# Kernel tuning notes

Measured on AMD Instinct MI355X. Metric: run time of the kernel, lower is better.

Reference implementation:

```python
import jax, jax.numpy as jnp
import numpy as np

D_MODEL = 1024
N_HEADS = 16
HEAD_DIM = D_MODEL // N_HEADS


def setup_inputs() -> dict:
    key = jax.random.key(0)
    k_x, k_wqkv, k_bqkv, k_wp, k_bp = jax.random.split(key, 5)
    B, N = 2, 2048
    x = jax.random.normal(k_x, (B, N, D_MODEL), dtype=jnp.float32)
    s = 1.0 / np.sqrt(D_MODEL)
    w_qkv = jax.random.uniform(k_wqkv, (D_MODEL, 3 * D_MODEL), jnp.float32, -s, s)
    b_qkv = jax.random.uniform(k_bqkv, (3 * D_MODEL,), jnp.float32, -s, s)
    w_proj = jax.random.uniform(k_wp, (D_MODEL, D_MODEL), jnp.float32, -s, s)
    b_proj = jax.random.uniform(k_bp, (D_MODEL,), jnp.float32, -s, s)
    return {"x": x, "w_qkv": w_qkv, "b_qkv": b_qkv, "w_proj": w_proj, "b_proj": b_proj}


def reference(x, w_qkv, b_qkv, w_proj, b_proj):
    B, N, C = x.shape
    scale = HEAD_DIM ** (-0.5)
    qkv = x @ w_qkv + b_qkv  # [B, N, 3C]
    qkv = qkv.reshape(B, N, 3, N_HEADS, HEAD_DIM).transpose(2, 0, 3, 1, 4)
    q, k, v = qkv[0], qkv[1], qkv[2]  # each [B, H, N, Dh]
    p = jnp.einsum('bhnd,bhmd->bhnm', q, k) * scale  # [B, H, N, N]
    p = jax.nn.softmax(p, axis=-1)
    o = jnp.einsum('bhnm,bhmd->bhnd', p, v)  # [B, H, N, Dh]
    o = o.transpose(0, 2, 1, 3).reshape(B, N, C)
    return o @ w_proj + b_proj
```

## Files before the change

### kernel.cpp

```cpp
#include <hip/hip_runtime.h>


typedef short v8s __attribute__((ext_vector_type(8)));
typedef float v4f __attribute__((ext_vector_type(4)));
typedef unsigned int v4u __attribute__((ext_vector_type(4)));

#define QSCALE 0.18033688011112042f

#if defined(__has_builtin)
# if __has_builtin(__builtin_amdgcn_exp2f)
#  define EXP2(x) __builtin_amdgcn_exp2f(x)
# endif
#endif
#ifndef EXP2
static __device__ __forceinline__ float exp2_asm(float x) {
    float r;
    asm volatile("v_exp_f32 %0, %1\n\ts_nop 1" : "=v"(r) : "v"(x));
    return r;
}
# define EXP2(x) exp2_asm(x)
#endif

static __device__ __forceinline__ unsigned short f2bf_fast(float f) {
    union { float f; unsigned int u; } a;
    a.f = f;
    return (unsigned short)((a.u + 0x8000u) >> 16);
}

static __device__ __forceinline__ unsigned int pack_bf16(float lo, float hi) {
    union { float f; unsigned int u; } a, b;
    a.f = lo; b.f = hi;
    return __builtin_amdgcn_perm(b.u + 0x8000u, a.u + 0x8000u, 0x07060302u);
}

#define GLD16(g, l) __builtin_amdgcn_global_load_lds( \
    (const __attribute__((address_space(1))) unsigned int*)(g), \
    (__attribute__((address_space(3))) unsigned int*)(l), 16, 0, 0)

__global__ __launch_bounds__(256) void prep(const float* __restrict__ x,
                                            unsigned short* __restrict__ xb,
                                            const float* __restrict__ w_qkv,
                                            unsigned short* __restrict__ wqkvt,
                                            const float* __restrict__ w_proj,
                                            unsigned short* __restrict__ wprojt) {
    __shared__ float tile[32][33];
    const int bid = blockIdx.x, tid = threadIdx.x;
    if (bid < 4096) {
        int i = bid * 256 + tid;
        float4 f = ((const float4*)x)[i];
        ushort4 o;
        o.x = f2bf_fast(f.x); o.y = f2bf_fast(f.y); o.z = f2bf_fast(f.z); o.w = f2bf_fast(f.w);
        ((ushort4*)xb)[i] = o;
        return;
    }
    const float* w; unsigned short* wt; int R, C, bx, by;
    if (bid < 7168) { w = w_qkv; wt = wqkvt; R = 1024; C = 3072;
                      int t = bid - 4096; bx = t % 96; by = t / 96; }
    else            { w = w_proj; wt = wprojt; R = 1024; C = 1024;
                      int t = bid - 7168; bx = t & 31; by = t >> 5; }
    const int tx = tid & 31, ty = tid >> 5;
    const int c0 = bx * 32, r0 = by * 32;
#pragma unroll
    for (int j = 0; j < 32; j += 8)
        tile[ty + j][tx] = w[(r0 + ty + j) * C + c0 + tx];
    __syncthreads();
#pragma unroll
    for (int j = 0; j < 32; j += 8)
        wt[(c0 + ty + j) * R + r0 + tx] = f2bf_fast(tile[tx][ty + j]);
}

__global__ __launch_bounds__(256) void gemm_bt(const unsigned short* __restrict__ A,
                                               const unsigned short* __restrict__ Bt,
                                               const float* __restrict__ bias,
                                               int M, int N, int K, int mode,
                                               unsigned short* __restrict__ qo,
                                               unsigned short* __restrict__ ko,
                                               unsigned short* __restrict__ vto,
                                               float* __restrict__ outp) {
    __shared__ unsigned short Sh[17408];
    const int tid = threadIdx.x;
    const int wave = tid >> 6, lane = tid & 63;
    const int quad = lane >> 4, l16 = lane & 15;
    const int bm = blockIdx.y * 128, bn = blockIdx.x * 128;
    const int wm = (wave >> 1) * 64, wn = (wave & 1) * 64;
    const int rsw = (quad ^ ((l16 >> 1) & 3)) << 3;

    v4f acc[4][4];
#pragma unroll
    for (int i = 0; i < 4; i++)
#pragma unroll
        for (int j = 0; j < 4; j++) acc[i][j] = (v4f){0.f, 0.f, 0.f, 0.f};

#define GSTAGE(b, kk) do { \
    _Pragma("unroll") \
    for (int i_ = 0; i_ < 2; i_++) { \
        int c_ = i_ * 256 + tid; \
        int r_ = c_ >> 2; \
        int g_ = ((c_ & 3) ^ ((r_ >> 1) & 3)) << 3; \
        GLD16(&A[(bm + r_) * K + (kk) + g_], &Sh[((b) << 12) + (c_ << 3)]); \
        GLD16(&Bt[(bn + r_) * K + (kk) + g_], &Sh[8192 + ((b) << 12) + (c_ << 3)]); \
    } } while (0)

#define GCOMP(b) do { \
    v8s af_[4], bf_[4]; \
    _Pragma("unroll") \
    for (int mi_ = 0; mi_ < 4; mi_++) \
        af_[mi_] = *(const v8s*)&Sh[((b) << 12) + (wm + mi_ * 16 + l16) * 32 + rsw]; \
    _Pragma("unroll") \
    for (int ni_ = 0; ni_ < 4; ni_++) \
        bf_[ni_] = *(const v8s*)&Sh[8192 + ((b) << 12) + (wn + ni_ * 16 + l16) * 32 + rsw]; \
    _Pragma("unroll") \
    for (int mi_ = 0; mi_ < 4; mi_++) \
        _Pragma("unroll") \
        for (int ni_ = 0; ni_ < 4; ni_++) \
            acc[mi_][ni_] = __builtin_amdgcn_mfma_f32_16x16x32_bf16( \
                af_[mi_], bf_[ni_], acc[mi_][ni_], 0, 0, 0); \
    } while (0)

    GSTAGE(0, 0);
    for (int k0 = 0; k0 < K; k0 += 64) {
        __syncthreads();
        if (k0 + 32 < K) GSTAGE(1, k0 + 32);
        GCOMP(0);
        __syncthreads();
        if (k0 + 64 < K) GSTAGE(0, k0 + 64);
        GCOMP(1);
    }
#undef GSTAGE
#undef GCOMP

    if (mode == 1) {
#pragma unroll
        for (int mi = 0; mi < 4; mi++)
#pragma unroll
            for (int ni = 0; ni < 4; ni++) {
                int col = bn + wn + ni * 16 + l16;
                float bv = bias[col];
                int row0 = bm + wm + mi * 16 + quad * 4;
#pragma unroll
                for (int r = 0; r < 4; r++)
                    outp[(row0 + r) * N + col] = acc[mi][ni][r] + bv;
            }
    } else if (bn < 2048) {
        const int isq = (bn < 1024);
        unsigned short* dst = isq ? qo : ko;
        const float sc = isq ? QSCALE : 1.0f;
#pragma unroll
        for (int mi = 0; mi < 4; mi++)
#pragma unroll
            for (int ni = 0; ni < 4; ni++) {
                int col = bn + wn + ni * 16 + l16;
                float bv = bias[col];
                int rem = col & 1023;
                int h = rem >> 6, dh = rem & 63;
                int row0 = bm + wm + mi * 16 + quad * 4;
                int b = row0 >> 11, n = row0 & 2047;
                unsigned short* p = &dst[(((b * 16 + h) << 11) + n) * 64 + dh];
                p[0]   = f2bf_fast((acc[mi][ni][0] + bv) * sc);
                p[64]  = f2bf_fast((acc[mi][ni][1] + bv) * sc);
                p[128] = f2bf_fast((acc[mi][ni][2] + bv) * sc);
                p[192] = f2bf_fast((acc[mi][ni][3] + bv) * sc);
            }
    } else {
        __syncthreads();
#pragma unroll
        for (int mi = 0; mi < 4; mi++)
#pragma unroll
            for (int ni = 0; ni < 4; ni++) {
                int col = bn + wn + ni * 16 + l16;
                float bv = bias[col];
                ushort4 pk;
                pk.x = f2bf_fast(acc[mi][ni][0] + bv);
                pk.y = f2bf_fast(acc[mi][ni][1] + bv);
                pk.z = f2bf_fast(acc[mi][ni][2] + bv);
                pk.w = f2bf_fast(acc[mi][ni][3] + bv);
                *(ushort4*)&Sh[(wn + ni * 16 + l16) * 136 +
                               wm + ((mi >> 1) * 32) + quad * 8 + ((mi & 1) * 4)] = pk;
            }
        __syncthreads();
        const int b = bm >> 11, n_base = bm & 2047;
#pragma unroll
        for (int j = 0; j < 8; j++) {
            int idx = j * 256 + tid;
            int Lcol = idx >> 4, rc = idx & 15;
            int rem = (bn + Lcol) & 1023;
            int h = rem >> 6, dh = rem & 63;
            *(int4*)&vto[((((b * 16 + h) * 64 + dh) << 11) + n_base + rc * 8)] =
                *(const int4*)&Sh[Lcol * 136 + rc * 8];
        }
    }
}

__global__ __launch_bounds__(256, 4) void attn(const unsigned short* __restrict__ q,
                                               const unsigned short* __restrict__ k,
                                               const unsigned short* __restrict__ vt,
                                               unsigned short* __restrict__ o) {
    __shared__ unsigned short Ks[2][64 * 64];
    __shared__ unsigned short Vs[2][64 * 64];
    const int tid = threadIdx.x;
    const int wave = tid >> 6, lane = tid & 63;
    const int quad = lane >> 4, l16 = lane & 15;
    const int sw = l16 & 7;

    const int id = blockIdx.y * 32 + blockIdx.x;
    const int bh = (id & 7) * 4 + ((id >> 3) & 3);
    const int wq0 = (id >> 5) * 64 + wave * 16;
    const int rowg = bh * 2048 + wq0;

    v8s qf[2];
#pragma unroll
    for (int half = 0; half < 2; half++)
        qf[half] = *(const v8s*)&q[(rowg + l16) * 64 + half * 32 + quad * 8];

    v8s onef;
#pragma unroll
    for (int j = 0; j < 8; j++) onef[j] = (short)0x3F80;

    v4f oacc[4];
    v4f lacc = (v4f){0.f, 0.f, 0.f, 0.f};
#pragma unroll
    for (int dt = 0; dt < 4; dt++) oacc[dt] = (v4f){0.f, 0.f, 0.f, 0.f};

    const unsigned short* kbase = k + (((long)bh << 11) * 64);
    const unsigned short* vbase = vt + (((long)bh * 64) << 11);

#define STAGE(buf, n0s) do { \
    _Pragma("unroll") \
    for (int i_ = 0; i_ < 2; i_++) { \
        int c_ = i_ * 256 + tid; \
        int r_ = c_ >> 3; \
        int chs_ = ((c_ & 7) ^ (r_ & 7)) << 3; \
        GLD16(&kbase[((n0s) + r_) * 64 + chs_], &Ks[buf][c_ << 3]); \
        GLD16(&vbase[(r_ << 11) + (n0s) + chs_], &Vs[buf][c_ << 3]); \
    } } while (0)

    auto tile = [&](const unsigned short* Kc, const unsigned short* Vc) {
        v4f s[4];
        __builtin_amdgcn_s_setprio(1);
#pragma unroll
        for (int ni = 0; ni < 4; ni++) {
            int rowk = (ni * 16 + l16) * 64;
            v8s kf0 = *(const v8s*)&Kc[rowk + ((quad ^ sw) << 3)];
            v8s kf1 = *(const v8s*)&Kc[rowk + (((4 + quad) ^ sw) << 3)];
            v4f z = (v4f){0.f, 0.f, 0.f, 0.f};
            z = __builtin_amdgcn_mfma_f32_16x16x32_bf16(kf0, qf[0], z, 0, 0, 0);
            z = __builtin_amdgcn_mfma_f32_16x16x32_bf16(kf1, qf[1], z, 0, 0, 0);
            s[ni] = z;
        }
        __builtin_amdgcn_s_setprio(0);

        v8s af[2];
#pragma unroll
        for (int t = 0; t < 2; t++) {
            v4u w;
            w[0] = pack_bf16(EXP2(s[2 * t][0]),     EXP2(s[2 * t][1]));
            w[1] = pack_bf16(EXP2(s[2 * t][2]),     EXP2(s[2 * t][3]));
            w[2] = pack_bf16(EXP2(s[2 * t + 1][0]), EXP2(s[2 * t + 1][1]));
            w[3] = pack_bf16(EXP2(s[2 * t + 1][2]), EXP2(s[2 * t + 1][3]));
            union { v4u u; v8s s8; } cv;
            cv.u = w;
            af[t] = cv.s8;
        }

        __builtin_amdgcn_s_setprio(1);
#pragma unroll
        for (int dt = 0; dt < 4; dt++) {
            int rowv = (dt * 16 + l16) * 64;
            v8s vf0 = *(const v8s*)&Vc[rowv + ((quad ^ sw) << 3)];
            v8s vf1 = *(const v8s*)&Vc[rowv + (((4 + quad) ^ sw) << 3)];
            oacc[dt] = __builtin_amdgcn_mfma_f32_16x16x32_bf16(af[0], vf0, oacc[dt], 0, 0, 0);
            oacc[dt] = __builtin_amdgcn_mfma_f32_16x16x32_bf16(af[1], vf1, oacc[dt], 0, 0, 0);
        }
        lacc = __builtin_amdgcn_mfma_f32_16x16x32_bf16(af[0], onef, lacc, 0, 0, 0);
        lacc = __builtin_amdgcn_mfma_f32_16x16x32_bf16(af[1], onef, lacc, 0, 0, 0);
        __builtin_amdgcn_s_setprio(0);
    };

    STAGE(0, 0);
    for (int n0 = 0; n0 < 2048; n0 += 128) {
        __syncthreads();
        if (n0 + 64 < 2048) STAGE(1, n0 + 64);
        tile(Ks[0], Vs[0]);
        __syncthreads();
        if (n0 + 128 < 2048) STAGE(0, n0 + 128);
        tile(Ks[1], Vs[1]);
    }
#undef STAGE

    const int b = bh >> 4, h = bh & 15;
#pragma unroll
    for (int r = 0; r < 4; r++) {
        float linv = 1.0f / lacc[r];
        int n = wq0 + quad * 4 + r;
#pragma unroll
        for (int dt = 0; dt < 4; dt++)
            o[(b * 2048 + n) * 1024 + h * 64 + dt * 16 + l16] =
                f2bf_fast(oacc[dt][r] * linv);
    }
}

extern "C" void kernel_launch(void* const* d_in, const int* in_sizes, int n_in,
                              void* d_out, int out_size, void* d_ws, size_t ws_size,
                              hipStream_t stream) {
    const float* x      = (const float*)d_in[0];
    const float* w_qkv  = (const float*)d_in[1];
    const float* b_qkv  = (const float*)d_in[2];
    const float* w_proj = (const float*)d_in[3];
    const float* b_proj = (const float*)d_in[4];
    float* outp = (float*)d_out;

    unsigned short* ws     = (unsigned short*)d_ws;
    unsigned short* xb     = ws;
    unsigned short* wqkvt  = ws + 4194304;
    unsigned short* wprojt = wqkvt + 3145728;
    unsigned short* qws    = wprojt + 1048576;
    unsigned short* kws    = qws + 4194304;
    unsigned short* vtws   = kws + 4194304;
    unsigned short* ows    = xb;

    prep<<<8192, 256, 0, stream>>>(x, xb, w_qkv, wqkvt, w_proj, wprojt);
    gemm_bt<<<dim3(24, 32), 256, 0, stream>>>(xb, wqkvt, b_qkv, 4096, 3072, 1024, 0,
                                              qws, kws, vtws, nullptr);
    attn<<<dim3(32, 32), 256, 0, stream>>>(qws, kws, vtws, ows);
    gemm_bt<<<dim3(8, 32), 256, 0, stream>>>(ows, wprojt, b_proj, 4096, 1024, 1024, 1,
                                             nullptr, nullptr, nullptr, outp);
}
```

Baseline: 183.5 us.

## Triple-buffer GEMM k-loop, swizzle block order, and stage Q/K epilogue through LDS

Replaces the two-stage double-buffered k-loop in gemm_bt with a three-buffer rotating pipeline that keeps two loads in flight, using explicit vmcnt waits and raw barriers instead of __syncthreads. It also remaps block IDs with a grouped swizzle to improve L2 reuse of A/B tiles. The Q/K epilogue now writes results to LDS first and then issues coalesced 16-byte stores to global memory instead of scattered 2-byte stores. In exchange, shared memory grows to 48KB, which may reduce occupancy, and the swizzle assumes the grid size divides evenly.

Measured after the change: 180.6 us. No clear change (-1.5%).

```diff
diff --git a/kernel.cpp b/kernel.cpp
--- a/kernel.cpp
+++ b/kernel.cpp
@@ -77,11 +77,14 @@
                                                unsigned short* __restrict__ ko,
                                                unsigned short* __restrict__ vto,
                                                float* __restrict__ outp) {
-    __shared__ unsigned short Sh[17408];
+    __shared__ unsigned short Sh[24576];
     const int tid = threadIdx.x;
     const int wave = tid >> 6, lane = tid & 63;
     const int quad = lane >> 4, l16 = lane & 15;
-    const int bm = blockIdx.y * 128, bn = blockIdx.x * 128;
+    const int W = gridDim.x;
+    const int id = blockIdx.y * W + blockIdx.x;
+    const int s = (id & 7) * (W << 2) + (id >> 3);
+    const int bm = (s / W) * 128, bn = (s % W) * 128;
     const int wm = (wave >> 1) * 64, wn = (wave & 1) * 64;
     const int rsw = (quad ^ ((l16 >> 1) & 3)) << 3;
 
@@ -91,24 +94,24 @@
 #pragma unroll
         for (int j = 0; j < 4; j++) acc[i][j] = (v4f){0.f, 0.f, 0.f, 0.f};
 
-#define GSTAGE(b, kk) do { \
+#define GSTAGE(off, kk) do { \
     _Pragma("unroll") \
     for (int i_ = 0; i_ < 2; i_++) { \
         int c_ = i_ * 256 + tid; \
         int r_ = c_ >> 2; \
         int g_ = ((c_ & 3) ^ ((r_ >> 1) & 3)) << 3; \
-        GLD16(&A[(bm + r_) * K + (kk) + g_], &Sh[((b) << 12) + (c_ << 3)]); \
-        GLD16(&Bt[(bn + r_) * K + (kk) + g_], &Sh[8192 + ((b) << 12) + (c_ << 3)]); \
+        GLD16(&A[(bm + r_) * K + (kk) + g_], &Sh[(off) + (c_ << 3)]); \
+        GLD16(&Bt[(bn + r_) * K + (kk) + g_], &Sh[(off) + 4096 + (c_ << 3)]); \
     } } while (0)
 
-#define GCOMP(b) do { \
+#define GCOMP(off) do { \
     v8s af_[4], bf_[4]; \
     _Pragma("unroll") \
     for (int mi_ = 0; mi_ < 4; mi_++) \
-        af_[mi_] = *(const v8s*)&Sh[((b) << 12) + (wm + mi_ * 16 + l16) * 32 + rsw]; \
+        af_[mi_] = *(const v8s*)&Sh[(off) + (wm + mi_ * 16 + l16) * 32 + rsw]; \
     _Pragma("unroll") \
     for (int ni_ = 0; ni_ < 4; ni_++) \
-        bf_[ni_] = *(const v8s*)&Sh[8192 + ((b) << 12) + (wn + ni_ * 16 + l16) * 32 + rsw]; \
+        bf_[ni_] = *(const v8s*)&Sh[(off) + 4096 + (wn + ni_ * 16 + l16) * 32 + rsw]; \
     _Pragma("unroll") \
     for (int mi_ = 0; mi_ < 4; mi_++) \
         _Pragma("unroll") \
@@ -117,15 +120,22 @@
                 af_[mi_], bf_[ni_], acc[mi_][ni_], 0, 0, 0); \
     } while (0)
 
-    GSTAGE(0, 0);
-    for (int k0 = 0; k0 < K; k0 += 64) {
-        __syncthreads();
-        if (k0 + 32 < K) GSTAGE(1, k0 + 32);
-        GCOMP(0);
-        __syncthreads();
-        if (k0 + 64 < K) GSTAGE(0, k0 + 64);
-        GCOMP(1);
-    }
+    const int nt = K >> 5;
+    int o0 = 0, o1 = 8192, o2 = 16384;
+    GSTAGE(o0, 0);
+    GSTAGE(o1, 32);
+    for (int t = 0; t < nt - 1; ++t) {
+        asm volatile("s_waitcnt vmcnt(4)" ::: "memory");
+        __builtin_amdgcn_s_barrier();
+        __builtin_amdgcn_sched_barrier(0);
+        if (t + 2 < nt) GSTAGE(o2, (t + 2) << 5);
+        GCOMP(o0);
+        int tmp = o0; o0 = o1; o1 = o2; o2 = tmp;
+    }
+    asm volatile("s_waitcnt vmcnt(0)" ::: "memory");
+    __builtin_amdgcn_s_barrier();
+    __builtin_amdgcn_sched_barrier(0);
+    GCOMP(o0);
 #undef GSTAGE
 #undef GCOMP
 
@@ -145,22 +155,29 @@
         const int isq = (bn < 1024);
         unsigned short* dst = isq ? qo : ko;
         const float sc = isq ? QSCALE : 1.0f;
+        __syncthreads();
 #pragma unroll
         for (int mi = 0; mi < 4; mi++)
 #pragma unroll
             for (int ni = 0; ni < 4; ni++) {
-                int col = bn + wn + ni * 16 + l16;
-                float bv = bias[col];
-                int rem = col & 1023;
-                int h = rem >> 6, dh = rem & 63;
-                int row0 = bm + wm + mi * 16 + quad * 4;
-                int b = row0 >> 11, n = row0 & 2047;
-                unsigned short* p = &dst[(((b * 16 + h) << 11) + n) * 64 + dh];
-                p[0]   = f2bf_fast((acc[mi][ni][0] + bv) * sc);
-                p[64]  = f2bf_fast((acc[mi][ni][1] + bv) * sc);
-                p[128] = f2bf_fast((acc[mi][ni][2] + bv) * sc);
-                p[192] = f2bf_fast((acc[mi][ni][3] + bv) * sc);
+                int c = wn + ni * 16 + l16;
+                float bv = bias[bn + c];
+                int r0 = wm + mi * 16 + quad * 4;
+#pragma unroll
+                for (int r = 0; r < 4; r++)
+                    Sh[(r0 + r) * 136 + c] = f2bf_fast((acc[mi][ni][r] + bv) * sc);
             }
+        __syncthreads();
+        const int bb = bm >> 11, nb = bm & 2047;
+#pragma unroll
+        for (int j = 0; j < 8; j++) {
+            int idx = j * 256 + tid;
+            int r = idx >> 4, c8 = idx & 15;
+            int rem = (bn + c8 * 8) & 1023;
+            int h = rem >> 6, dh = rem & 63;
+            *(int4*)&dst[(((bb * 16 + h) << 11) + nb + r) * 64 + dh] =
+                *(const int4*)&Sh[r * 136 + c8 * 8];
+        }
     } else {
         __syncthreads();
 #pragma unroll
```
